# Kernel optimization log

Hardware: AMD Instinct MI355X
Metric: run time of the kernel (lower is better)

Reference implementation:

```python
import jax, jax.numpy as jnp
import numpy as np

L, B, D_IN, D = 96, 32, 4, 128   # leaves, batch, input feats, dim_feedforward
NB, NC = 3, 6                    # n_blocks, n_classes
E = L * (L - 1)                  # directed edges, no self-loops


def _adjacency():
    # one-hot receiver/sender matrices, shape (E, L)
    pairs = np.array([(i, j) for i in range(L) for j in range(L) if i != j])
    recv, send = pairs[:, 0], pairs[:, 1]
    rr = np.zeros((E, L), np.float32); rr[np.arange(E), recv] = 1.0
    rs = np.zeros((E, L), np.float32); rs[np.arange(E), send] = 1.0
    return rr, rs


def setup_inputs() -> dict:
    key = jax.random.key(0)
    ks = jax.random.split(key, 24)
    rr, rs = _adjacency()
    inp = {
        'inputs': jax.random.normal(ks[0], (L, B, D_IN), jnp.float32),
        'rel_rec': jnp.broadcast_to(jnp.asarray(rr), (B, E, L)),
        'rel_send': jnp.broadcast_to(jnp.asarray(rs), (B, E, L)),
    }
    s = 0.1
    # initial MLP: D_IN -> D -> D
    inp['W0a'] = s * jax.random.normal(ks[1], (D_IN, D)); inp['b0a'] = jnp.zeros((D,))
    inp['W0b'] = s * jax.random.normal(ks[2], (D, D));    inp['b0b'] = jnp.zeros((D,))
    # per-block edge MLP (2D -> D -> D) and node MLP (D -> D -> D), stacked over NB
    inp['eW1'] = s * jax.random.normal(ks[3], (NB, 2 * D, D)); inp['eb1'] = jnp.zeros((NB, D))
    inp['eW2'] = s * jax.random.normal(ks[4], (NB, D, D));     inp['eb2'] = jnp.zeros((NB, D))
    inp['nW1'] = s * jax.random.normal(ks[5], (NB, D, D));     inp['nb1'] = jnp.zeros((NB, D))
    inp['nW2'] = s * jax.random.normal(ks[6], (NB, D, D));     inp['nb2'] = jnp.zeros((NB, D))
    # final MLP: 2D -> D -> NC
    inp['fW1'] = s * jax.random.normal(ks[7], (2 * D, D)); inp['fb1'] = jnp.zeros((D,))
    inp['fW2'] = s * jax.random.normal(ks[8], (D, NC));    inp['fb2'] = jnp.zeros((NC,))
    return inp


def _mlp(x, W1, b1, W2, b2):
    return jax.nn.elu(jax.nn.elu(x @ W1 + b1) @ W2 + b2)


def reference(inputs, rel_rec, rel_send, W0a, b0a, W0b, b0b,
              eW1, eb1, eW2, eb2, nW1, nb1, nW2, nb2,
              fW1, fb1, fW2, fb2):
    def node2edge(h):
        # (b,l,d) -> (b,E,2d): cat([senders, receivers])
        senders = jnp.einsum('bel,bld->bed', rel_send, h)
        receivers = jnp.einsum('bel,bld->bed', rel_rec, h)
        return jnp.concatenate([senders, receivers], axis=2)

    def edge2node(h):
        # (b,E,d) -> (b,l,d), mean over incoming edges
        incoming = jnp.einsum('bel,bed->bld', rel_rec, h)
        denom = rel_rec.sum(1)[:, 1]  # (b,)
        return incoming / denom[:, None, None]

    x = jnp.transpose(inputs, (1, 0, 2))           # (b, l, d_in)
    x = _mlp(x, W0a, b0a, W0b, b0b)                # (b, l, D)
    x = node2edge(x)                               # (b, E, 2D)
    for i in range(NB):
        x = _mlp(x, eW1[i], eb1[i], eW2[i], eb2[i])  # (b, E, D)
        x = edge2node(x)                             # (b, l, D)
        x = _mlp(x, nW1[i], nb1[i], nW2[i], nb2[i])  # (b, l, D)
        x = node2edge(x)                             # (b, E, 2D)
    out = jax.nn.elu(x @ fW1 + fb1) @ fW2 + fb2    # (b, E, NC)
    return out
```

## Files before the change

### kernel.cpp

```cpp
#include <hip/hip_runtime.h>
#include <hip/hip_bf16.h>

#define LN 96
#define BN 32
#define DM 128
#define EPN 95

typedef __attribute__((ext_vector_type(8))) short s16x8;
typedef __attribute__((ext_vector_type(4))) float f32x4;

__device__ __forceinline__ float eluf(float x){ return x > 0.f ? x : __expf(x) - 1.f; }
__device__ __forceinline__ unsigned short f2bf(float f){
    unsigned u = __float_as_uint(f);
    return (unsigned short)((u + 0x7fff + ((u >> 16) & 1)) >> 16);
}
__device__ __forceinline__ float bf2f(unsigned short h){ return __uint_as_float(((unsigned)h) << 16); }

struct SrcTab { const float* p[19]; };

__global__ void conv_pack_kernel(SrcTab tab, unsigned short* __restrict__ hi,
                                 unsigned short* __restrict__ lo){
    int tid = blockIdx.x * 256 + threadIdx.x;
    int m = tid >> 11, c = tid & 2047;
    int l = c & 63, f = c >> 6;
    int n = (f >> 2) * 16 + (l & 15);
    int k0 = (f & 3) * 32 + (l >> 4) * 8;
    union { unsigned short us[8]; uint4 v; } ph, pl;
#pragma unroll
    for (int e = 0; e < 8; ++e){
        float x;
        if (m == 18) x = (n < 6) ? tab.p[18][(k0 + e) * 6 + n] : 0.f;
        else         x = tab.p[m][(k0 + e) * DM + n];
        unsigned short h = f2bf(x);
        ph.us[e] = h;
        pl.us[e] = f2bf(x - bf2f(h));
    }
    *(uint4*)(hi + (size_t)tid * 8) = ph.v;
    *(uint4*)(lo + (size_t)tid * 8) = pl.v;
}

__device__ __forceinline__ void mmw(const char* atile, int l,
                                    const unsigned short* __restrict__ whW,
                                    const unsigned short* __restrict__ wlW,
                                    f32x4 acc[2]) {
    const int l15 = l & 15, kgrp = l >> 4;
    s16x8 a[4];
#pragma unroll
    for (int ks = 0; ks < 4; ++ks)
        a[ks] = *(const s16x8*)(atile + ((l15 * 256 + (ks * 32 + kgrp * 8) * 2) ^ ((l15 & 7) << 4)));
#pragma unroll
    for (int ntl = 0; ntl < 2; ++ntl) {
#pragma unroll
        for (int ks = 0; ks < 4; ++ks) {
            s16x8 bh = *(const s16x8*)(whW + (size_t)((ntl * 4 + ks) * 64 + l) * 8);
            acc[ntl] = __builtin_amdgcn_mfma_f32_16x16x32_bf16(a[ks], bh, acc[ntl], 0, 0, 0);
        }
#pragma unroll
        for (int ks = 0; ks < 4; ++ks) {
            s16x8 bl = *(const s16x8*)(wlW + (size_t)((ntl * 4 + ks) * 64 + l) * 8);
            acc[ntl] = __builtin_amdgcn_mfma_f32_16x16x32_bf16(a[ks], bl, acc[ntl], 0, 0, 0);
        }
    }
}

__device__ __forceinline__ void store_act(char* atile, int l, int w, f32x4 acc[2]) {
    const int l15 = l & 15, kgrp = l >> 4;
#pragma unroll
    for (int ntl = 0; ntl < 2; ++ntl)
#pragma unroll
        for (int i = 0; i < 4; ++i) {
            int row = kgrp * 4 + i;
            int col = (2 * w + ntl) * 16 + l15;
            *(unsigned short*)(atile + ((row * 256 + col * 2) ^ ((row & 7) << 4))) = f2bf(eluf(acc[ntl][i]));
        }
}

__global__ __launch_bounds__(256) void node0_kernel(
    const float* __restrict__ in,
    const float* __restrict__ W0a, const float* __restrict__ b0a,
    const unsigned short* __restrict__ w2h, const unsigned short* __restrict__ w2l,
    const float* __restrict__ b2,
    const unsigned short* __restrict__ wsh, const unsigned short* __restrict__ wsl,
    const unsigned short* __restrict__ wrh, const unsigned short* __restrict__ wrl,
    const float* __restrict__ bp,
    float* __restrict__ hs, float* __restrict__ hr) {
    __shared__ char atile[16 * 256];
    const int t = threadIdx.x;
    const int row0 = blockIdx.x * 16;
    const int l = t & 63, w = t >> 6;
    const int l15 = l & 15, kgrp = l >> 4;

    {
        int rr = t >> 4, q = t & 15, c0 = q * 8;
        int swz = (rr & 7) << 4;
        union { unsigned short us[8]; uint4 v; } pk;
        int row = row0 + rr;
        int b = row / LN, ll = row - b * LN;
        float4 x = *(const float4*)(in + (size_t)(ll * BN + b) * 4);
#pragma unroll
        for (int j = 0; j < 8; ++j) {
            int cc = c0 + j;
            float a = b0a[cc] + x.x * W0a[cc] + x.y * W0a[DM + cc]
                    + x.z * W0a[2 * DM + cc] + x.w * W0a[3 * DM + cc];
            pk.us[j] = f2bf(eluf(a));
        }
        *(uint4*)(atile + ((rr * 256 + c0 * 2) ^ swz)) = pk.v;
    }
    __syncthreads();

    f32x4 acc[2];
    const int cA = (2 * w) * 16 + l15, cB = (2 * w + 1) * 16 + l15;
    {
        float ba = b2[cA], bb = b2[cB];
        acc[0] = (f32x4){ba, ba, ba, ba};
        acc[1] = (f32x4){bb, bb, bb, bb};
        mmw(atile, l, w2h + w * 4096, w2l + w * 4096, acc);
        __syncthreads();
        store_act(atile, l, w, acc);
        __syncthreads();
    }
    acc[0] = (f32x4){0.f, 0.f, 0.f, 0.f};
    acc[1] = (f32x4){0.f, 0.f, 0.f, 0.f};
    mmw(atile, l, wsh + w * 4096, wsl + w * 4096, acc);
#pragma unroll
    for (int ntl = 0; ntl < 2; ++ntl)
#pragma unroll
        for (int i = 0; i < 4; ++i)
            hs[(size_t)(row0 + kgrp * 4 + i) * DM + (2 * w + ntl) * 16 + l15] = acc[ntl][i];
    {
        float ba = bp[cA], bb = bp[cB];
        acc[0] = (f32x4){ba, ba, ba, ba};
        acc[1] = (f32x4){bb, bb, bb, bb};
        mmw(atile, l, wrh + w * 4096, wrl + w * 4096, acc);
    }
#pragma unroll
    for (int ntl = 0; ntl < 2; ++ntl)
#pragma unroll
        for (int i = 0; i < 4; ++i)
            hr[(size_t)(row0 + kgrp * 4 + i) * DM + (2 * w + ntl) * 16 + l15] = acc[ntl][i];
}

__global__ __launch_bounds__(256) void edge_node_kernel(
    const float* __restrict__ hsIn, const float* __restrict__ hrIn,
    const unsigned short* __restrict__ whi, const unsigned short* __restrict__ wlo,
    int eslot, const float* __restrict__ eb2v,
    int s1, int s2, int sS,
    const float* __restrict__ b1, const float* __restrict__ b2, const float* __restrict__ bp,
    float* __restrict__ hsOut, float* __restrict__ hrOut) {
    __shared__ char y1[LN * 256];
    __shared__ float hrL[4 * DM];
    __shared__ float gL[4 * DM];
    __shared__ char actA[16 * 256];
    __shared__ char actB[16 * 256];
    const int blk = blockIdx.x;
    const int b = blk / 24, r0 = (blk % 24) * 4;
    const int t = threadIdx.x;
    const int w = t >> 6, l = t & 63;
    const int l15 = l & 15, kgrp = l >> 4;

    if (t < 128) {
        int rr = t >> 5, c4 = (t & 31) * 4;
        *(float4*)(hrL + rr * DM + c4) = *(const float4*)(hrIn + ((size_t)(b * LN + r0 + rr)) * DM + c4);
    }
    s16x8 bfr[2][4];
#pragma unroll
    for (int ntl = 0; ntl < 2; ++ntl)
#pragma unroll
        for (int ks = 0; ks < 4; ++ks)
            bfr[ntl][ks] = *(const s16x8*)(whi + (size_t)eslot * 16384 +
                           (size_t)(((2 * w + ntl) * 4 + ks) * 64 + l) * 8);
    float b20 = eb2v[(2 * w) * 16 + l15], b21 = eb2v[(2 * w + 1) * 16 + l15];
    __syncthreads();

    const float* hsB = hsIn + (size_t)(b * LN) * DM;
    for (int rr4 = 0; rr4 < 4; ++rr4) {
        int r = r0 + rr4;
#pragma unroll
        for (int rep = 0; rep < 6; ++rep) {
            int task = t + rep * 256;
            int rr = task >> 4, c0 = (task & 15) * 8;
            int swz = (rr & 7) << 4;
            union { unsigned short us[8]; uint4 v; } pk;
            if (rr < EPN) {
                int j = rr + (rr >= r);
                const float* hp = hsB + (size_t)j * DM + c0;
                const float* rp = hrL + rr4 * DM + c0;
                f32x4 h0 = *(const f32x4*)hp, h1 = *(const f32x4*)(hp + 4);
                f32x4 v0 = *(const f32x4*)rp, v1 = *(const f32x4*)(rp + 4);
#pragma unroll
                for (int e = 0; e < 4; ++e) {
                    pk.us[e]     = f2bf(eluf(h0[e] + v0[e]));
                    pk.us[e + 4] = f2bf(eluf(h1[e] + v1[e]));
                }
            } else pk.v = make_uint4(0, 0, 0, 0);
            *(uint4*)(y1 + ((rr * 256 + c0 * 2) ^ swz)) = pk.v;
        }
        __syncthreads();
        f32x4 acc[6][2] = {};
#pragma unroll
        for (int mt = 0; mt < 6; ++mt) {
            int arow = mt * 16 + l15;
            const char* rb = y1 + arow * 256;
            int swz = (arow & 7) << 4;
#pragma unroll
            for (int ks = 0; ks < 4; ++ks) {
                s16x8 a = *(const s16x8*)(rb + (((ks * 32 + kgrp * 8) * 2) ^ swz));
                acc[mt][0] = __builtin_amdgcn_mfma_f32_16x16x32_bf16(a, bfr[0][ks], acc[mt][0], 0, 0, 0);
                acc[mt][1] = __builtin_amdgcn_mfma_f32_16x16x32_bf16(a, bfr[1][ks], acc[mt][1], 0, 0, 0);
            }
        }
        float cs0 = 0.f, cs1 = 0.f;
#pragma unroll
        for (int mt = 0; mt < 6; ++mt)
#pragma unroll
            for (int i = 0; i < 4; ++i) {
                int row = mt * 16 + kgrp * 4 + i;
                if (row < EPN) {
                    cs0 += eluf(acc[mt][0][i] + b20);
                    cs1 += eluf(acc[mt][1][i] + b21);
                }
            }
        cs0 += __shfl_xor(cs0, 16); cs0 += __shfl_xor(cs0, 32);
        cs1 += __shfl_xor(cs1, 16); cs1 += __shfl_xor(cs1, 32);
        if (l < 16) {
            gL[rr4 * DM + (2 * w) * 16 + l]       = cs0 * (1.f / 95.f);
            gL[rr4 * DM + (2 * w + 1) * 16 + l]   = cs1 * (1.f / 95.f);
        }
        __syncthreads();
    }

    {
        int rr = t >> 4, q = t & 15, c0 = q * 8;
        int swz = (rr & 7) << 4;
        union { unsigned short us[8]; uint4 v; } pk;
        if (rr < 4) {
            const float* src = gL + rr * DM + c0;
            float4 f0 = *(const float4*)(src);
            float4 f1 = *(const float4*)(src + 4);
            pk.us[0] = f2bf(f0.x); pk.us[1] = f2bf(f0.y); pk.us[2] = f2bf(f0.z); pk.us[3] = f2bf(f0.w);
            pk.us[4] = f2bf(f1.x); pk.us[5] = f2bf(f1.y); pk.us[6] = f2bf(f1.z); pk.us[7] = f2bf(f1.w);
        } else pk.v = make_uint4(0, 0, 0, 0);
        *(uint4*)(actA + ((rr * 256 + c0 * 2) ^ swz)) = pk.v;
    }
    __syncthreads();

    f32x4 acc[2];
    const int cA = (2 * w) * 16 + l15, cB = (2 * w + 1) * 16 + l15;
    {
        float ba = b1[cA], bb = b1[cB];
        acc[0] = (f32x4){ba, ba, ba, ba};
        acc[1] = (f32x4){bb, bb, bb, bb};
        mmw(actA, l, whi + (size_t)s1 * 16384 + w * 4096, wlo + (size_t)s1 * 16384 + w * 4096, acc);
        __syncthreads();
        store_act(actB, l, w, acc);
        __syncthreads();
    }
    {
        float ba = b2[cA], bb = b2[cB];
        acc[0] = (f32x4){ba, ba, ba, ba};
        acc[1] = (f32x4){bb, bb, bb, bb};
        mmw(actB, l, whi + (size_t)s2 * 16384 + w * 4096, wlo + (size_t)s2 * 16384 + w * 4096, acc);
        __syncthreads();
        store_act(actA, l, w, acc);
        __syncthreads();
    }
    acc[0] = (f32x4){0.f, 0.f, 0.f, 0.f};
    acc[1] = (f32x4){0.f, 0.f, 0.f, 0.f};
    mmw(actA, l, whi + (size_t)sS * 16384 + w * 4096, wlo + (size_t)sS * 16384 + w * 4096, acc);
#pragma unroll
    for (int ntl = 0; ntl < 2; ++ntl)
#pragma unroll
        for (int i = 0; i < 4; ++i) {
            int row = kgrp * 4 + i;
            if (row < 4)
                hsOut[(size_t)(b * LN + r0 + row) * DM + (2 * w + ntl) * 16 + l15] = acc[ntl][i];
        }
    {
        float ba = bp[cA], bb = bp[cB];
        acc[0] = (f32x4){ba, ba, ba, ba};
        acc[1] = (f32x4){bb, bb, bb, bb};
        mmw(actA, l, whi + (size_t)(sS + 1) * 16384 + w * 4096, wlo + (size_t)(sS + 1) * 16384 + w * 4096, acc);
    }
#pragma unroll
    for (int ntl = 0; ntl < 2; ++ntl)
#pragma unroll
        for (int i = 0; i < 4; ++i) {
            int row = kgrp * 4 + i;
            if (row < 4)
                hrOut[(size_t)(b * LN + r0 + row) * DM + (2 * w + ntl) * 16 + l15] = acc[ntl][i];
        }
}

__global__ void final_kernel(const float* __restrict__ hs, const float* __restrict__ hr,
                             const float* __restrict__ fW2, const float* __restrict__ fb2,
                             float* __restrict__ out) {
    __shared__ float w2l[DM * 6];
    __shared__ float hrbuf[DM];
    const int r = blockIdx.x, b = blockIdx.y;
    const int t = threadIdx.x;
    hrbuf[t] = hr[((size_t)b * LN + r) * DM + t];
    for (int c = 0; c < 6; ++c) w2l[t * 6 + c] = fW2[t * 6 + c];
    __syncthreads();
    int k = t;
    if (k < EPN) {
        int j = k + (k >= r);
        const float* src = hs + ((size_t)b * LN + j) * DM;
        float acc[6];
        for (int c = 0; c < 6; ++c) acc[c] = fb2[c];
        for (int d0 = 0; d0 < DM; d0 += 4) {
            float4 f = *(const float4*)(src + d0);
            float v0 = eluf(f.x + hrbuf[d0 + 0]);
            float v1 = eluf(f.y + hrbuf[d0 + 1]);
            float v2 = eluf(f.z + hrbuf[d0 + 2]);
            float v3 = eluf(f.w + hrbuf[d0 + 3]);
            for (int c = 0; c < 6; ++c)
                acc[c] += v0 * w2l[(d0 + 0) * 6 + c] + v1 * w2l[(d0 + 1) * 6 + c]
                        + v2 * w2l[(d0 + 2) * 6 + c] + v3 * w2l[(d0 + 3) * 6 + c];
        }
        float* o = out + (((size_t)b * (LN * EPN)) + r * EPN + k) * 6;
        for (int c = 0; c < 6; ++c) o[c] = acc[c];
    }
}

extern "C" void kernel_launch(void* const* d_in, const int* in_sizes, int n_in,
                              void* d_out, int out_size, void* d_ws, size_t ws_size,
                              hipStream_t stream) {
    const float* inputs = (const float*)d_in[0];
    const float* W0a = (const float*)d_in[3];
    const float* b0a = (const float*)d_in[4];
    const float* W0b = (const float*)d_in[5];
    const float* b0b = (const float*)d_in[6];
    const float* eW1 = (const float*)d_in[7];
    const float* eb1 = (const float*)d_in[8];
    const float* eW2 = (const float*)d_in[9];
    const float* eb2 = (const float*)d_in[10];
    const float* nW1 = (const float*)d_in[11];
    const float* nb1 = (const float*)d_in[12];
    const float* nW2 = (const float*)d_in[13];
    const float* nb2 = (const float*)d_in[14];
    const float* fW1 = (const float*)d_in[15];
    const float* fb1 = (const float*)d_in[16];
    const float* fW2 = (const float*)d_in[17];
    const float* fb2 = (const float*)d_in[18];
    float* out = (float*)d_out;

    const int NR = BN * LN;
    unsigned short* whi = (unsigned short*)d_ws;
    unsigned short* wlo = whi + 19 * 16384;
    float* hsA = (float*)(wlo + 19 * 16384);
    float* hrA = hsA + NR * DM;
    float* hsB = hrA + NR * DM;
    float* hrB = hsB + NR * DM;

    SrcTab tab;
    tab.p[0] = eW2;          tab.p[1] = eW2 + 16384;  tab.p[2] = eW2 + 32768;
    tab.p[3] = W0b;
    tab.p[4] = eW1;          tab.p[5] = eW1 + 16384;
    tab.p[6] = nW1;          tab.p[7] = nW2;          tab.p[8] = eW1 + 32768;  tab.p[9]  = eW1 + 49152;
    tab.p[10] = nW1 + 16384; tab.p[11] = nW2 + 16384; tab.p[12] = eW1 + 65536; tab.p[13] = eW1 + 81920;
    tab.p[14] = nW1 + 32768; tab.p[15] = nW2 + 32768; tab.p[16] = fW1;         tab.p[17] = fW1 + 16384;
    tab.p[18] = fW2;

    #define WM(m) (whi + (m) * 16384), (wlo + (m) * 16384)

    conv_pack_kernel<<<152, 256, 0, stream>>>(tab, whi, wlo);
    node0_kernel<<<192, 256, 0, stream>>>(inputs, W0a, b0a, WM(3), b0b, WM(4), WM(5), eb1, hsA, hrA);
    edge_node_kernel<<<768, 256, 0, stream>>>(hsA, hrA, whi, wlo, 0, eb2,
                                              6, 7, 8, nb1, nb2, eb1 + DM, hsB, hrB);
    edge_node_kernel<<<768, 256, 0, stream>>>(hsB, hrB, whi, wlo, 1, eb2 + DM,
                                              10, 11, 12, nb1 + DM, nb2 + DM, eb1 + 2 * DM, hsA, hrA);
    edge_node_kernel<<<768, 256, 0, stream>>>(hsA, hrA, whi, wlo, 2, eb2 + 2 * DM,
                                              14, 15, 16, nb1 + 2 * DM, nb2 + 2 * DM, fb1, hsB, hrB);
    final_kernel<<<dim3(LN, BN), 128, 0, stream>>>(hsB, hrB, fW2, fb2, out);
    #undef WM
}
```

Baseline: 142.1 us.

## Regrid edge kernel to 3 rows per block, batch-minor block order, packed bf16 cvt

The edge/node kernel now handles 3 receiver rows per block instead of 4, giving 1024 blocks instead of 768 for better load balance across CUs. Block indices are reordered so consecutive blocks cover different batches, and node0 and final kernels get a matching remap that changes which blocks run together and share cache. The y1 staging loop issues global loads for two tasks before converting, and uses the v_cvt_pk_bf16_f32 instruction instead of manual rounding. Per-row overhead of loading the weight fragments and running the node MLP is now amortized over fewer rows.

```diff
diff --git a/kernel.cpp b/kernel.cpp
--- a/kernel.cpp
+++ b/kernel.cpp
@@ -15,6 +15,11 @@
     return (unsigned short)((u + 0x7fff + ((u >> 16) & 1)) >> 16);
 }
 __device__ __forceinline__ float bf2f(unsigned short h){ return __uint_as_float(((unsigned)h) << 16); }
+__device__ __forceinline__ unsigned cvtpk(float lo, float hi){
+    unsigned r;
+    asm("v_cvt_pk_bf16_f32 %0, %1, %2" : "=v"(r) : "v"(lo), "v"(hi));
+    return r;
+}
 
 struct SrcTab { const float* p[19]; };
 
@@ -86,12 +91,13 @@
     float* __restrict__ hs, float* __restrict__ hr) {
     __shared__ char atile[16 * 256];
     const int t = threadIdx.x;
-    const int row0 = blockIdx.x * 16;
+    const int q = blockIdx.x >> 5, bblk = blockIdx.x & 31;
+    const int row0 = bblk * LN + q * 16;
     const int l = t & 63, w = t >> 6;
     const int l15 = l & 15, kgrp = l >> 4;
 
     {
-        int rr = t >> 4, q = t & 15, c0 = q * 8;
+        int rr = t >> 4, qq = t & 15, c0 = qq * 8;
         int swz = (rr & 7) << 4;
         union { unsigned short us[8]; uint4 v; } pk;
         int row = row0 + rr;
@@ -148,17 +154,18 @@
     const float* __restrict__ b1, const float* __restrict__ b2, const float* __restrict__ bp,
     float* __restrict__ hsOut, float* __restrict__ hrOut) {
     __shared__ char y1[LN * 256];
-    __shared__ float hrL[4 * DM];
-    __shared__ float gL[4 * DM];
+    __shared__ float hrL[3 * DM];
+    __shared__ float gL[3 * DM];
     __shared__ char actA[16 * 256];
     __shared__ char actB[16 * 256];
     const int blk = blockIdx.x;
-    const int b = blk / 24, r0 = (blk % 24) * 4;
+    const int rg = blk >> 5, b = blk & 31;
+    const int r0 = rg * 3;
     const int t = threadIdx.x;
     const int w = t >> 6, l = t & 63;
     const int l15 = l & 15, kgrp = l >> 4;
 
-    if (t < 128) {
+    if (t < 96) {
         int rr = t >> 5, c4 = (t & 31) * 4;
         *(float4*)(hrL + rr * DM + c4) = *(const float4*)(hrIn + ((size_t)(b * LN + r0 + rr)) * DM + c4);
     }
@@ -173,27 +180,41 @@
     __syncthreads();
 
     const float* hsB = hsIn + (size_t)(b * LN) * DM;
-    for (int rr4 = 0; rr4 < 4; ++rr4) {
-        int r = r0 + rr4;
-#pragma unroll
-        for (int rep = 0; rep < 6; ++rep) {
-            int task = t + rep * 256;
-            int rr = task >> 4, c0 = (task & 15) * 8;
-            int swz = (rr & 7) << 4;
-            union { unsigned short us[8]; uint4 v; } pk;
-            if (rr < EPN) {
-                int j = rr + (rr >= r);
-                const float* hp = hsB + (size_t)j * DM + c0;
-                const float* rp = hrL + rr4 * DM + c0;
-                f32x4 h0 = *(const f32x4*)hp, h1 = *(const f32x4*)(hp + 4);
-                f32x4 v0 = *(const f32x4*)rp, v1 = *(const f32x4*)(rp + 4);
-#pragma unroll
-                for (int e = 0; e < 4; ++e) {
-                    pk.us[e]     = f2bf(eluf(h0[e] + v0[e]));
-                    pk.us[e + 4] = f2bf(eluf(h1[e] + v1[e]));
+    for (int rr3 = 0; rr3 < 3; ++rr3) {
+        int r = r0 + rr3;
+#pragma unroll
+        for (int ch = 0; ch < 3; ++ch) {
+            float4 h0[2], h1[2];
+            int rrs[2], c0s[2];
+#pragma unroll
+            for (int k = 0; k < 2; ++k) {
+                int task = t + (ch * 2 + k) * 256;
+                int rr = task >> 4, c0 = (task & 15) * 8;
+                rrs[k] = rr; c0s[k] = c0;
+                if (rr < EPN) {
+                    int j = rr + (rr >= r);
+                    const float* hp = hsB + (size_t)j * DM + c0;
+                    h0[k] = *(const float4*)hp;
+                    h1[k] = *(const float4*)(hp + 4);
                 }
-            } else pk.v = make_uint4(0, 0, 0, 0);
-            *(uint4*)(y1 + ((rr * 256 + c0 * 2) ^ swz)) = pk.v;
+            }
+#pragma unroll
+            for (int k = 0; k < 2; ++k) {
+                int rr = rrs[k], c0 = c0s[k];
+                int swz = (rr & 7) << 4;
+                uint4 pk = make_uint4(0, 0, 0, 0);
+                if (rr < EPN) {
+                    const float* rp = hrL + rr3 * DM + c0;
+                    f32x4 v0 = *(const f32x4*)rp, v1 = *(const f32x4*)(rp + 4);
+                    float e0 = eluf(h0[k].x + v0[0]), e1 = eluf(h0[k].y + v0[1]);
+                    float e2 = eluf(h0[k].z + v0[2]), e3 = eluf(h0[k].w + v0[3]);
+                    float e4 = eluf(h1[k].x + v1[0]), e5 = eluf(h1[k].y + v1[1]);
+                    float e6 = eluf(h1[k].z + v1[2]), e7 = eluf(h1[k].w + v1[3]);
+                    pk.x = cvtpk(e0, e1); pk.y = cvtpk(e2, e3);
+                    pk.z = cvtpk(e4, e5); pk.w = cvtpk(e6, e7);
+                }
+                *(uint4*)(y1 + ((rr * 256 + c0 * 2) ^ swz)) = pk;
+            }
         }
         __syncthreads();
         f32x4 acc[6][2] = {};
@@ -223,8 +244,8 @@
         cs0 += __shfl_xor(cs0, 16); cs0 += __shfl_xor(cs0, 32);
         cs1 += __shfl_xor(cs1, 16); cs1 += __shfl_xor(cs1, 32);
         if (l < 16) {
-            gL[rr4 * DM + (2 * w) * 16 + l]       = cs0 * (1.f / 95.f);
-            gL[rr4 * DM + (2 * w + 1) * 16 + l]   = cs1 * (1.f / 95.f);
+            gL[rr3 * DM + (2 * w) * 16 + l]     = cs0 * (1.f / 95.f);
+            gL[rr3 * DM + (2 * w + 1) * 16 + l] = cs1 * (1.f / 95.f);
         }
         __syncthreads();
     }
@@ -233,7 +254,7 @@
         int rr = t >> 4, q = t & 15, c0 = q * 8;
         int swz = (rr & 7) << 4;
         union { unsigned short us[8]; uint4 v; } pk;
-        if (rr < 4) {
+        if (rr < 3) {
             const float* src = gL + rr * DM + c0;
             float4 f0 = *(const float4*)(src);
             float4 f1 = *(const float4*)(src + 4);
@@ -272,7 +293,7 @@
 #pragma unroll
         for (int i = 0; i < 4; ++i) {
             int row = kgrp * 4 + i;
-            if (row < 4)
+            if (row < 3)
                 hsOut[(size_t)(b * LN + r0 + row) * DM + (2 * w + ntl) * 16 + l15] = acc[ntl][i];
         }
     {
@@ -286,7 +307,7 @@
 #pragma unroll
         for (int i = 0; i < 4; ++i) {
             int row = kgrp * 4 + i;
-            if (row < 4)
+            if (row < 3)
                 hrOut[(size_t)(b * LN + r0 + row) * DM + (2 * w + ntl) * 16 + l15] = acc[ntl][i];
         }
 }
@@ -296,7 +317,7 @@
                              float* __restrict__ out) {
     __shared__ float w2l[DM * 6];
     __shared__ float hrbuf[DM];
-    const int r = blockIdx.x, b = blockIdx.y;
+    const int b = blockIdx.x, r = blockIdx.y;
     const int t = threadIdx.x;
     hrbuf[t] = hr[((size_t)b * LN + r) * DM + t];
     for (int c = 0; c < 6; ++c) w2l[t * 6 + c] = fW2[t * 6 + c];
@@ -365,12 +386,12 @@
 
     conv_pack_kernel<<<152, 256, 0, stream>>>(tab, whi, wlo);
     node0_kernel<<<192, 256, 0, stream>>>(inputs, W0a, b0a, WM(3), b0b, WM(4), WM(5), eb1, hsA, hrA);
-    edge_node_kernel<<<768, 256, 0, stream>>>(hsA, hrA, whi, wlo, 0, eb2,
-                                              6, 7, 8, nb1, nb2, eb1 + DM, hsB, hrB);
-    edge_node_kernel<<<768, 256, 0, stream>>>(hsB, hrB, whi, wlo, 1, eb2 + DM,
-                                              10, 11, 12, nb1 + DM, nb2 + DM, eb1 + 2 * DM, hsA, hrA);
-    edge_node_kernel<<<768, 256, 0, stream>>>(hsA, hrA, whi, wlo, 2, eb2 + 2 * DM,
-                                              14, 15, 16, nb1 + 2 * DM, nb2 + 2 * DM, fb1, hsB, hrB);
-    final_kernel<<<dim3(LN, BN), 128, 0, stream>>>(hsB, hrB, fW2, fb2, out);
+    edge_node_kernel<<<1024, 256, 0, stream>>>(hsA, hrA, whi, wlo, 0, eb2,
+                                               6, 7, 8, nb1, nb2, eb1 + DM, hsB, hrB);
+    edge_node_kernel<<<1024, 256, 0, stream>>>(hsB, hrB, whi, wlo, 1, eb2 + DM,
+                                               10, 11, 12, nb1 + DM, nb2 + DM, eb1 + 2 * DM, hsA, hrA);
+    edge_node_kernel<<<1024, 256, 0, stream>>>(hsA, hrA, whi, wlo, 2, eb2 + 2 * DM,
+                                               14, 15, 16, nb1 + 2 * DM, nb2 + 2 * DM, fb1, hsB, hrB);
+    final_kernel<<<dim3(BN, LN), 128, 0, stream>>>(hsB, hrB, fW2, fb2, out);
     #undef WM
 }
```

Result: faster. 138.0 us (-2.9%).
